# Kernel tuning notes

Hardware: AMD Instinct MI355X
Metric: run time of the kernel (lower is better)

## Reference

```python
import jax, jax.numpy as jnp
import numpy as np

HEADS = 8
EPS = 1e-5


def layernorm(x, g, b):
    mu = jnp.mean(x, axis=-1, keepdims=True)
    var = jnp.mean((x - mu) ** 2, axis=-1, keepdims=True)
    return (x - mu) * jax.lax.rsqrt(var + EPS) * g + b


def setup_inputs() -> dict:
    key = jax.random.key(0)
    ks = jax.random.split(key, 5)
    B, C, H, W = 8, 384, 32, 32
    d = C
    s = 0.02
    return {
        "x": jax.random.normal(ks[0], (B, C, H, W), jnp.float32),
        "ln1_g": jnp.ones((d,), jnp.float32),
        "ln1_b": jnp.zeros((d,), jnp.float32),
        "lna_g": jnp.ones((d,), jnp.float32),
        "lna_b": jnp.zeros((d,), jnp.float32),
        "w_qkv": jax.random.normal(ks[1], (d, 3 * d), jnp.float32) * s,
        "w_out": jax.random.normal(ks[2], (d, d), jnp.float32) * s,
        "ln2_g": jnp.ones((d,), jnp.float32),
        "ln2_b": jnp.zeros((d,), jnp.float32),
        "w1": jax.random.normal(ks[3], (d, 4 * d), jnp.float32) * s,
        "b1": jnp.zeros((4 * d,), jnp.float32),
        "w2": jax.random.normal(ks[4], (4 * d, d), jnp.float32) * s,
        "b2": jnp.zeros((d,), jnp.float32),
    }


def reference(x, ln1_g, ln1_b, lna_g, lna_b, w_qkv, w_out, ln2_g, ln2_b, w1, b1, w2, b2):
    B, C, H, W = x.shape
    d = C
    dh = d // HEADS
    scale = dh ** (-0.5)
    # flatten spatial -> tokens: [B, N, C]
    t = x.reshape(B, C, H * W).transpose(0, 2, 1)

    # --- attention branch (note: double pre-norm, as in original) ---
    a = layernorm(t, ln1_g, ln1_b)
    a = layernorm(a, lna_g, lna_b)
    qkv = a @ w_qkv  # [B, N, 3d]
    q, k, v = jnp.split(qkv, 3, axis=-1)
    q = q.reshape(B, -1, HEADS, dh).transpose(0, 2, 1, 3)  # b h n d
    k = k.reshape(B, -1, HEADS, dh).transpose(0, 2, 1, 3)
    v = v.reshape(B, -1, HEADS, dh).transpose(0, 2, 1, 3)
    dots = jnp.einsum("bhnd,bhmd->bhnm", q, k) * scale
    attn = jax.nn.softmax(dots, axis=-1)
    o = jnp.einsum("bhnm,bhmd->bhnd", attn, v)
    o = o.transpose(0, 2, 1, 3).reshape(B, -1, d)
    t = t + o @ w_out

    # --- MLP branch (exact GELU, as torch nn.GELU default) ---
    m = layernorm(t, ln2_g, ln2_b)
    m = jax.nn.gelu(m @ w1 + b1, approximate=False) @ w2 + b2
    t = t + m

    return t.transpose(0, 2, 1).reshape(B, C, H, W)
```

## Files before the change

kernel.cpp:

```cpp
#include <hip/hip_runtime.h>
#include <math.h>

#define NTOK 1024
#define DM   384
#define NHEAD 8
#define DH   48
#define BATCH 8
#define NROWS (BATCH * NTOK)
#define SC2   (0.14433756729740643f * 1.4426950408889634f)

typedef __attribute__((ext_vector_type(8))) _Float16 f16x8;
typedef __attribute__((ext_vector_type(2))) __fp16 fp16x2_raw;
typedef __attribute__((ext_vector_type(4))) float f32x4;

#define ASYNC16(gp, lp) __builtin_amdgcn_global_load_lds( \
    (const __attribute__((address_space(1))) void*)(gp),  \
    (__attribute__((address_space(3))) void*)(lp), 16, 0, 0)

#define EXP2R(x) __builtin_amdgcn_exp2f(x)
#define RCPR(x)  __builtin_amdgcn_rcpf(x)

__device__ __forceinline__ unsigned int pkh(float a, float b) {
    union { fp16x2_raw h; unsigned int u; } cv;
    cv.h = __builtin_amdgcn_cvt_pkrtz(a, b);
    return cv.u;
}

__device__ __forceinline__ float gelu_fast(float v) {
    const float u = v * (0.7978845608f + 0.0356774081f * v * v);
    const float e = EXP2R(fminf(u * 2.885390082f, 120.0f));
    return v * e * RCPR(e + 1.0f);
}

__global__ __launch_bounds__(256) void prep_kernel(const float* __restrict__ x,
                                                   const float* __restrict__ ln1_g,
                                                   const float* __restrict__ ln1_b,
                                                   const float* __restrict__ lna_g,
                                                   const float* __restrict__ lna_b,
                                                   float* __restrict__ t,
                                                   _Float16* __restrict__ a_h,
                                                   const float* __restrict__ wqkv,
                                                   const float* __restrict__ wout,
                                                   const float* __restrict__ w1,
                                                   const float* __restrict__ w2,
                                                   _Float16* __restrict__ wqkvT,
                                                   _Float16* __restrict__ woutT,
                                                   _Float16* __restrict__ w1T,
                                                   _Float16* __restrict__ w2T) {
    __shared__ float Ts[32][389];
    const int bid = blockIdx.x;
    const int tid = threadIdx.x;

    if (bid >= 256) {
        float (*tile)[33] = (float(*)[33])&Ts[0][0];
        const int wb = bid - 256;
        const float* W; _Float16* Wt; int K, N, nx, tt;
        if (wb < 432)       { W = wqkv; Wt = wqkvT; K = 384;  N = 1152; nx = 36; tt = wb; }
        else if (wb < 576)  { W = wout; Wt = woutT; K = 384;  N = 384;  nx = 12; tt = wb - 432; }
        else if (wb < 1152) { W = w1;   Wt = w1T;   K = 384;  N = 1536; nx = 48; tt = wb - 576; }
        else                { W = w2;   Wt = w2T;   K = 1536; N = 384;  nx = 12; tt = wb - 1152; }
        const int n0 = (tt % nx) * 32, k0 = (tt / nx) * 32;
        const int tx = tid & 31, ty = tid >> 5;
        #pragma unroll
        for (int i = ty; i < 32; i += 8)
            tile[i][tx] = W[(size_t)(k0 + i) * N + n0 + tx];
        __syncthreads();
        #pragma unroll
        for (int i = ty; i < 32; i += 8)
            Wt[(size_t)(n0 + i) * K + k0 + tx] = (_Float16)tile[tx][i];
        return;
    }

    const int b = bid >> 5, n0 = (bid & 31) * 32;
    const int tx = tid & 31, ty8 = tid >> 5;
    const float* xb = x + (size_t)b * (DM * NTOK);
    #pragma unroll
    for (int c0 = 0; c0 < DM; c0 += 32) {
        #pragma unroll
        for (int i = ty8; i < 32; i += 8)
            Ts[tx][c0 + i] = xb[(size_t)(c0 + i) * NTOK + n0 + tx];
    }
    __syncthreads();

    const int g = tid >> 3, sub = tid & 7;
    const int c0 = sub * 48;
    float xv[48];
    #pragma unroll
    for (int k = 0; k < 12; ++k)
        *(float4*)&xv[k * 4] = *(const float4*)&Ts[g][c0 + k * 4];

    const size_t trow = (size_t)((b << 10) + n0 + g) * DM;
    float s = 0.0f, sq = 0.0f;
    #pragma unroll
    for (int k = 0; k < 12; ++k)
        *(float4*)&t[trow + c0 + k * 4] = *(const float4*)&xv[k * 4];
    #pragma unroll
    for (int j = 0; j < 48; ++j) { s += xv[j]; sq += xv[j] * xv[j]; }
    s += __shfl_xor(s, 1, 64); sq += __shfl_xor(sq, 1, 64);
    s += __shfl_xor(s, 2, 64); sq += __shfl_xor(sq, 2, 64);
    s += __shfl_xor(s, 4, 64); sq += __shfl_xor(sq, 4, 64);
    float mu = s * (1.0f / DM);
    float var = fmaxf(sq * (1.0f / DM) - mu * mu, 0.0f);
    float r1 = rsqrtf(var + 1e-5f);

    float s2 = 0.0f, q2 = 0.0f;
    #pragma unroll
    for (int k = 0; k < 12; ++k) {
        const float4 gk = *(const float4*)&ln1_g[c0 + k * 4];
        const float4 bk = *(const float4*)&ln1_b[c0 + k * 4];
        float y0 = (xv[k*4+0] - mu) * r1 * gk.x + bk.x;
        float y1 = (xv[k*4+1] - mu) * r1 * gk.y + bk.y;
        float y2 = (xv[k*4+2] - mu) * r1 * gk.z + bk.z;
        float y3 = (xv[k*4+3] - mu) * r1 * gk.w + bk.w;
        xv[k*4+0] = y0; xv[k*4+1] = y1; xv[k*4+2] = y2; xv[k*4+3] = y3;
        s2 += (y0 + y1) + (y2 + y3);
        q2 += (y0*y0 + y1*y1) + (y2*y2 + y3*y3);
    }
    s2 += __shfl_xor(s2, 1, 64); q2 += __shfl_xor(q2, 1, 64);
    s2 += __shfl_xor(s2, 2, 64); q2 += __shfl_xor(q2, 2, 64);
    s2 += __shfl_xor(s2, 4, 64); q2 += __shfl_xor(q2, 4, 64);
    mu = s2 * (1.0f / DM);
    var = fmaxf(q2 * (1.0f / DM) - mu * mu, 0.0f);
    const float r2 = rsqrtf(var + 1e-5f);

    unsigned int d[12];
    #pragma unroll
    for (int k = 0; k < 12; ++k) {
        const float4 gk = *(const float4*)&lna_g[c0 + k * 4];
        const float4 bk = *(const float4*)&lna_b[c0 + k * 4];
        const float y0 = (xv[k*4+0] - mu) * r2 * gk.x + bk.x;
        const float y1 = (xv[k*4+1] - mu) * r2 * gk.y + bk.y;
        const float y2 = (xv[k*4+2] - mu) * r2 * gk.z + bk.z;
        const float y3 = (xv[k*4+3] - mu) * r2 * gk.w + bk.w;
        d[k*2+0] = pkh(y0, y1); d[k*2+1] = pkh(y2, y3);
    }
    unsigned int* op = (unsigned int*)(a_h + trow + c0);
    #pragma unroll
    for (int k = 0; k < 3; ++k)
        *(uint4*)(op + k * 4) = *(const uint4*)&d[k * 4];
}

template <int EPI, int BN>
__global__ __launch_bounds__(256, 2) void gemm_f16(const _Float16* __restrict__ A,
                                                   const _Float16* __restrict__ Bt,
                                                   const float* __restrict__ bias,
                                                   const float* __restrict__ R,
                                                   _Float16* __restrict__ Ch,
                                                   float* __restrict__ Cf,
                                                   int M, int N, int K) {
    constexpr int NFRAG = BN / 32;
    __shared__ _Float16 As[2][128][64];
    __shared__ _Float16 Bs[2][BN][64];
    const int tid = threadIdx.x;
    const int w = tid >> 6, lane = tid & 63;
    const int l15 = lane & 15, lq = lane >> 4;
    const int bm = blockIdx.y * 128, bn = blockIdx.x * BN;
    const int moff = (w & 1) * 64, noff = (w >> 1) * (BN / 2);

    const int srw = lane >> 3, pp = lane & 7;
    const int c = pp ^ srw;
    const _Float16* Ag[4];
    const _Float16* Bg[NFRAG];
    #pragma unroll
    for (int j = 0; j < 4; ++j)
        Ag[j] = A + (size_t)(bm + w * 32 + j * 8 + srw) * K + c * 8;
    #pragma unroll
    for (int j = 0; j < NFRAG; ++j)
        Bg[j] = Bt + (size_t)(bn + w * (BN / 4) + j * 8 + srw) * K + c * 8;

    const int octA = ((lq ^ (l15 & 7)) << 4);

    f32x4 acc[4][NFRAG];
    #pragma unroll
    for (int mi = 0; mi < 4; ++mi)
        #pragma unroll
        for (int ni = 0; ni < NFRAG; ++ni) acc[mi][ni] = (f32x4){0.f, 0.f, 0.f, 0.f};

    #pragma unroll
    for (int j = 0; j < 4; ++j) { ASYNC16(Ag[j], &As[0][w * 32 + j * 8][0]); Ag[j] += 64; }
    #pragma unroll
    for (int j = 0; j < NFRAG; ++j) { ASYNC16(Bg[j], &Bs[0][w * (BN / 4) + j * 8][0]); Bg[j] += 64; }

    const int nkt = K >> 6;
    for (int kt = 0; kt < nkt; ++kt) {
        const int cur = kt & 1;
        __syncthreads();
        if (kt < nkt - 1) {
            #pragma unroll
            for (int j = 0; j < 4; ++j) { ASYNC16(Ag[j], &As[cur ^ 1][w * 32 + j * 8][0]); Ag[j] += 64; }
            #pragma unroll
            for (int j = 0; j < NFRAG; ++j) { ASYNC16(Bg[j], &Bs[cur ^ 1][w * (BN / 4) + j * 8][0]); Bg[j] += 64; }
        }
        const char* Ab = (const char*)&As[cur][0][0];
        const char* Bb = (const char*)&Bs[cur][0][0];
        #pragma unroll
        for (int ks = 0; ks < 2; ++ks) {
            const int ox = octA ^ (ks << 6);
            f16x8 af[4], bfr[NFRAG];
            #pragma unroll
            for (int mi = 0; mi < 4; ++mi)
                af[mi] = *(const f16x8*)(Ab + ((moff + mi * 16 + l15) << 7) + ox);
            #pragma unroll
            for (int ni = 0; ni < NFRAG; ++ni)
                bfr[ni] = *(const f16x8*)(Bb + ((noff + ni * 16 + l15) << 7) + ox);
            #pragma unroll
            for (int mi = 0; mi < 4; ++mi)
                #pragma unroll
                for (int ni = 0; ni < NFRAG; ++ni)
                    acc[mi][ni] = __builtin_amdgcn_mfma_f32_16x16x32_f16(af[mi], bfr[ni], acc[mi][ni], 0, 0, 0);
        }
    }

    #pragma unroll
    for (int mi = 0; mi < 4; ++mi) {
        #pragma unroll
        for (int ni = 0; ni < NFRAG; ++ni) {
            const int col = bn + noff + ni * 16 + l15;
            float bv = 0.0f;
            if (EPI >= 2) bv = bias[col];
            if (EPI == 4) {
                const int row0 = bm + moff + mi * 16 + lq * 4;
                const int b = row0 >> 10, nn = row0 & 1023;
                float4 vv;
                vv.x = acc[mi][ni][0] + bv + R[(size_t)(row0 + 0) * N + col];
                vv.y = acc[mi][ni][1] + bv + R[(size_t)(row0 + 1) * N + col];
                vv.z = acc[mi][ni][2] + bv + R[(size_t)(row0 + 2) * N + col];
                vv.w = acc[mi][ni][3] + bv + R[(size_t)(row0 + 3) * N + col];
                *(float4*)(Cf + (size_t)b * (DM * NTOK) + (size_t)col * NTOK + nn) = vv;
            } else {
                #pragma unroll
                for (int r = 0; r < 4; ++r) {
                    const int row = bm + moff + mi * 16 + lq * 4 + r;
                    const size_t idx = (size_t)row * N + col;
                    float v = acc[mi][ni][r];
                    if (EPI == 2) v = gelu_fast(v + bv);
                    Ch[idx] = (_Float16)v;
                }
            }
        }
    }
}

__global__ __launch_bounds__(256) void gemm_out_ln(const _Float16* __restrict__ A,
                                                   const _Float16* __restrict__ Bt,
                                                   float* __restrict__ T,
                                                   _Float16* __restrict__ a_out,
                                                   const float* __restrict__ gg,
                                                   const float* __restrict__ bb) {
    __shared__ _Float16 As[2][32][64];
    __shared__ _Float16 Bs[2][384][64];
    __shared__ float red_s[4][16];
    __shared__ float red_q[4][16];
    const int tid = threadIdx.x;
    const int w = tid >> 6, lane = tid & 63;
    const int l15 = lane & 15, lq = lane >> 4;
    const int bm = blockIdx.x * 32;
    const int mr = (w & 1) * 16;
    const int cq = (w >> 1) * 192;

    const int srw = lane >> 3, pp = lane & 7;
    const int c = pp ^ srw;
    const _Float16* Ag = A + (size_t)(bm + w * 8 + srw) * 384 + c * 8;
    const _Float16* Bg[12];
    #pragma unroll
    for (int j = 0; j < 12; ++j)
        Bg[j] = Bt + (size_t)(j * 32 + w * 8 + srw) * 384 + c * 8;

    const int octA = ((lq ^ (l15 & 7)) << 4);

    f32x4 acc[12];
    #pragma unroll
    for (int ni = 0; ni < 12; ++ni) acc[ni] = (f32x4){0.f, 0.f, 0.f, 0.f};

    ASYNC16(Ag, &As[0][w * 8][0]); Ag += 64;
    #pragma unroll
    for (int j = 0; j < 12; ++j) { ASYNC16(Bg[j], &Bs[0][j * 32 + w * 8][0]); Bg[j] += 64; }

    for (int kt = 0; kt < 6; ++kt) {
        const int cur = kt & 1;
        __syncthreads();
        if (kt < 5) {
            ASYNC16(Ag, &As[cur ^ 1][w * 8][0]); Ag += 64;
            #pragma unroll
            for (int j = 0; j < 12; ++j) { ASYNC16(Bg[j], &Bs[cur ^ 1][j * 32 + w * 8][0]); Bg[j] += 64; }
        }
        #pragma unroll
        for (int ks = 0; ks < 2; ++ks) {
            const int ox = octA ^ (ks << 6);
            const f16x8 af = *(const f16x8*)((const char*)&As[cur][0][0] + ((mr + l15) << 7) + ox);
            #pragma unroll
            for (int ni = 0; ni < 12; ++ni) {
                const f16x8 bf = *(const f16x8*)((const char*)&Bs[cur][0][0] + ((cq + ni * 16 + l15) << 7) + ox);
                acc[ni] = __builtin_amdgcn_mfma_f32_16x16x32_f16(af, bf, acc[ni], 0, 0, 0);
            }
        }
    }

    float vv[12][4];
    float s[4] = {0.f, 0.f, 0.f, 0.f}, q[4] = {0.f, 0.f, 0.f, 0.f};
    #pragma unroll
    for (int ni = 0; ni < 12; ++ni) {
        const int col = cq + ni * 16 + l15;
        #pragma unroll
        for (int r = 0; r < 4; ++r) {
            const int row = bm + mr + lq * 4 + r;
            const float v = acc[ni][r] + T[(size_t)row * DM + col];
            vv[ni][r] = v;
            T[(size_t)row * DM + col] = v;
            s[r] += v; q[r] += v * v;
        }
    }
    #pragma unroll
    for (int off = 1; off < 16; off <<= 1) {
        #pragma unroll
        for (int r = 0; r < 4; ++r) {
            s[r] += __shfl_xor(s[r], off, 64);
            q[r] += __shfl_xor(q[r], off, 64);
        }
    }
    if (l15 == 0) {
        #pragma unroll
        for (int r = 0; r < 4; ++r) {
            red_s[w][lq * 4 + r] = s[r];
            red_q[w][lq * 4 + r] = q[r];
        }
    }
    __syncthreads();
    float mu[4], rs[4];
    #pragma unroll
    for (int r = 0; r < 4; ++r) {
        const float ts = s[r] + red_s[w ^ 2][lq * 4 + r];
        const float tq = q[r] + red_q[w ^ 2][lq * 4 + r];
        mu[r] = ts * (1.0f / DM);
        const float var = fmaxf(tq * (1.0f / DM) - mu[r] * mu[r], 0.0f);
        rs[r] = rsqrtf(var + 1e-5f);
    }
    #pragma unroll
    for (int ni = 0; ni < 12; ++ni) {
        const int col = cq + ni * 16 + l15;
        const float gv = gg[col], bv = bb[col];
        #pragma unroll
        for (int r = 0; r < 4; ++r) {
            const int row = bm + mr + lq * 4 + r;
            a_out[(size_t)row * DM + col] = (_Float16)((vv[ni][r] - mu[r]) * rs[r] * gv + bv);
        }
    }
}

__global__ __launch_bounds__(256) void attn_kernel(const _Float16* __restrict__ qkv,
                                                   _Float16* __restrict__ o) {
    __shared__ _Float16 Ks[2][64][64];
    __shared__ _Float16 Vt[2][48][72];
    __shared__ _Float16 Ps[4][16][72];
    const int tid = threadIdx.x;
    const int w = tid >> 6, lane = tid & 63;
    const int l15 = lane & 15, lq = lane >> 4;
    const int bid = blockIdx.x;
    const int bh = ((bid >> 3) & 7) * 8 + (bid & 7);
    const int qt0 = (bid >> 6) * 64;
    const int h = bh & 7, b = bh >> 3;

    const _Float16* qbase = qkv + (size_t)b * NTOK * 1152 + h * 48;
    const _Float16* kbase = qbase + 384;
    const _Float16* vbase = qbase + 768;

    f16x8 qf[2];
    {
        const size_t qrow = (size_t)(qt0 + w * 16 + l15) * 1152;
        qf[0] = *(const f16x8*)(qbase + qrow + lq * 8);
        if (lq < 2) qf[1] = *(const f16x8*)(qbase + qrow + 32 + lq * 8);
        else        qf[1] = (f16x8){(_Float16)0, (_Float16)0, (_Float16)0, (_Float16)0,
                                    (_Float16)0, (_Float16)0, (_Float16)0, (_Float16)0};
    }

    const int srw = lane >> 3, pp = lane & 7;
    const int ck = pp ^ srw;
    const int ckoff = (ck < 6) ? ck * 8 : (ck - 6) * 8;
    const _Float16* Kg = kbase + (size_t)(w * 16 + srw) * 1152 + ckoff;
    const int vtp = tid & 31, vfo = tid >> 5;
    const _Float16* Vg = vbase + (size_t)(vtp * 2) * 1152 + vfo * 8;

    const int octK = ((lq ^ (l15 & 7)) << 4);

    ASYNC16(Kg, &Ks[0][w * 16][0]);
    ASYNC16(Kg + 8 * 1152, &Ks[0][w * 16 + 8][0]);
    Kg += 64 * 1152;
    uint4 va, vb;
    if (vfo < 6) { va = *(const uint4*)Vg; vb = *(const uint4*)(Vg + 1152); }
    Vg += 64 * 1152;

    f32x4 oacc[3];
    float lpart = 0.0f;
    #pragma unroll
    for (int vf = 0; vf < 3; ++vf) oacc[vf] = (f32x4){0.f, 0.f, 0.f, 0.f};

    int cur = 0;
    for (int kt = 0; kt < 16; ++kt) {
        if (vfo < 6) {
            const unsigned short* as = (const unsigned short*)&va;
            const unsigned short* bs = (const unsigned short*)&vb;
            #pragma unroll
            for (int j = 0; j < 8; ++j) {
                const unsigned int dw = (unsigned int)as[j] | ((unsigned int)bs[j] << 16);
                *(unsigned int*)((char*)&Vt[cur][0][0] + (vfo * 8 + j) * 144 + vtp * 4) = dw;
            }
        }
        __syncthreads();
        if (kt < 15) {
            ASYNC16(Kg, &Ks[cur ^ 1][w * 16][0]);
            ASYNC16(Kg + 8 * 1152, &Ks[cur ^ 1][w * 16 + 8][0]);
            Kg += 64 * 1152;
            if (vfo < 6) { va = *(const uint4*)Vg; vb = *(const uint4*)(Vg + 1152); }
            Vg += 64 * 1152;
        }

        f32x4 sacc[4];
        #pragma unroll
        for (int mi = 0; mi < 4; ++mi) sacc[mi] = (f32x4){0.f, 0.f, 0.f, 0.f};
        #pragma unroll
        for (int ks = 0; ks < 2; ++ks) {
            const int ox = octK ^ (ks << 6);
            #pragma unroll
            for (int mi = 0; mi < 4; ++mi) {
                const f16x8 kf = *(const f16x8*)((const char*)&Ks[cur][0][0] + ((mi * 16 + l15) << 7) + ox);
                sacc[mi] = __builtin_amdgcn_mfma_f32_16x16x32_f16(kf, qf[ks], sacc[mi], 0, 0, 0);
            }
        }

        #pragma unroll
        for (int mi = 0; mi < 4; ++mi) {
            const float p0 = EXP2R(sacc[mi][0] * SC2);
            const float p1 = EXP2R(sacc[mi][1] * SC2);
            const float p2 = EXP2R(sacc[mi][2] * SC2);
            const float p3 = EXP2R(sacc[mi][3] * SC2);
            lpart += (p0 + p1) + (p2 + p3);
            uint2 d;
            d.x = pkh(p0, p1); d.y = pkh(p2, p3);
            *(uint2*)((char*)&Ps[w][0][0] + l15 * 144 + (mi * 16 + lq * 4) * 2) = d;
        }
        asm volatile("s_waitcnt lgkmcnt(0)" ::: "memory");

        #pragma unroll
        for (int ks = 0; ks < 2; ++ks) {
            const int kk2 = ks * 64 + lq * 16;
            const f16x8 pf = *(const f16x8*)((const char*)&Ps[w][0][0] + l15 * 144 + kk2);
            #pragma unroll
            for (int vf = 0; vf < 3; ++vf) {
                const f16x8 vv = *(const f16x8*)((const char*)&Vt[cur][0][0] + (vf * 16 + l15) * 144 + kk2);
                oacc[vf] = __builtin_amdgcn_mfma_f32_16x16x32_f16(vv, pf, oacc[vf], 0, 0, 0);
            }
        }
        cur ^= 1;
    }

    lpart += __shfl_xor(lpart, 16, 64);
    lpart += __shfl_xor(lpart, 32, 64);
    const float linv = RCPR(lpart);
    _Float16* ob = o + (size_t)(b * NTOK + qt0 + w * 16 + l15) * DM + h * DH;
    #pragma unroll
    for (int vf = 0; vf < 3; ++vf) {
        uint2 d;
        d.x = pkh(oacc[vf][0] * linv, oacc[vf][1] * linv);
        d.y = pkh(oacc[vf][2] * linv, oacc[vf][3] * linv);
        *(uint2*)(ob + vf * 16 + lq * 4) = d;
    }
}

extern "C" void kernel_launch(void* const* d_in, const int* in_sizes, int n_in,
                              void* d_out, int out_size, void* d_ws, size_t ws_size,
                              hipStream_t stream) {
    const float* x     = (const float*)d_in[0];
    const float* ln1_g = (const float*)d_in[1];
    const float* ln1_b = (const float*)d_in[2];
    const float* lna_g = (const float*)d_in[3];
    const float* lna_b = (const float*)d_in[4];
    const float* w_qkv = (const float*)d_in[5];
    const float* w_out = (const float*)d_in[6];
    const float* ln2_g = (const float*)d_in[7];
    const float* ln2_b = (const float*)d_in[8];
    const float* w1    = (const float*)d_in[9];
    const float* b1    = (const float*)d_in[10];
    const float* w2    = (const float*)d_in[11];
    const float* b2    = (const float*)d_in[12];
    float* out = (float*)d_out;

    char* wsb = (char*)d_ws;
    float* t          = (float*)(wsb);
    _Float16* a_h     = (_Float16*)(wsb + 12582912);
    _Float16* qkv_h   = (_Float16*)(wsb + 18874368);
    _Float16* o_h     = (_Float16*)(wsb + 37748736);
    _Float16* h1_h    = (_Float16*)(wsb + 44040192);
    _Float16* wqkvT   = (_Float16*)(wsb + 69206016);
    _Float16* woutT   = (_Float16*)(wsb + 70090752);
    _Float16* w1T     = (_Float16*)(wsb + 70385664);
    _Float16* w2T     = (_Float16*)(wsb + 71565312);

    prep_kernel<<<256 + 1728, 256, 0, stream>>>(x, ln1_g, ln1_b, lna_g, lna_b, t, a_h,
                                                w_qkv, w_out, w1, w2, wqkvT, woutT, w1T, w2T);
    gemm_f16<0, 192><<<dim3(6, 64), 256, 0, stream>>>(a_h, wqkvT, nullptr, nullptr, qkv_h, nullptr, NROWS, 3 * DM, DM);
    attn_kernel<<<1024, 256, 0, stream>>>(qkv_h, o_h);
    gemm_out_ln<<<256, 256, 0, stream>>>(o_h, woutT, t, a_h, ln2_g, ln2_b);
    gemm_f16<2, 192><<<dim3(8, 64), 256, 0, stream>>>(a_h, w1T, b1, nullptr, h1_h, nullptr, NROWS, 4 * DM, DM);
    gemm_f16<4, 64><<<dim3(6, 64), 256, 0, stream>>>(h1_h, w2T, b2, t, nullptr, out, NROWS, DM, 4 * DM);
}
```

Measured before the change: 219.3 us.

## Fuse out-projection, LayerNorm and full MLP into one tail kernel

Replaces the out-projection+LN kernel and the two MLP GEMM launches with a single kernel. Each 32-row block keeps the normalized activations and a 384-wide GELU hidden chunk in LDS and accumulates the down-projection in registers. This removes the global write and read of the hidden activation and the t residual round trip, plus two launches. In exchange, every block re-streams all of W1 and W2 with a small M tile and uses large LDS, which limits occupancy to one block per CU.

```diff
diff --git a/kernel.cpp b/kernel.cpp
--- a/kernel.cpp
+++ b/kernel.cpp
@@ -140,13 +140,10 @@
         *(uint4*)(op + k * 4) = *(const uint4*)&d[k * 4];
 }
 
-template <int EPI, int BN>
+template <int BN>
 __global__ __launch_bounds__(256, 2) void gemm_f16(const _Float16* __restrict__ A,
                                                    const _Float16* __restrict__ Bt,
-                                                   const float* __restrict__ bias,
-                                                   const float* __restrict__ R,
                                                    _Float16* __restrict__ Ch,
-                                                   float* __restrict__ Cf,
                                                    int M, int N, int K) {
     constexpr int NFRAG = BN / 32;
     __shared__ _Float16 As[2][128][64];
@@ -216,73 +213,65 @@
         #pragma unroll
         for (int ni = 0; ni < NFRAG; ++ni) {
             const int col = bn + noff + ni * 16 + l15;
-            float bv = 0.0f;
-            if (EPI >= 2) bv = bias[col];
-            if (EPI == 4) {
-                const int row0 = bm + moff + mi * 16 + lq * 4;
-                const int b = row0 >> 10, nn = row0 & 1023;
-                float4 vv;
-                vv.x = acc[mi][ni][0] + bv + R[(size_t)(row0 + 0) * N + col];
-                vv.y = acc[mi][ni][1] + bv + R[(size_t)(row0 + 1) * N + col];
-                vv.z = acc[mi][ni][2] + bv + R[(size_t)(row0 + 2) * N + col];
-                vv.w = acc[mi][ni][3] + bv + R[(size_t)(row0 + 3) * N + col];
-                *(float4*)(Cf + (size_t)b * (DM * NTOK) + (size_t)col * NTOK + nn) = vv;
-            } else {
-                #pragma unroll
-                for (int r = 0; r < 4; ++r) {
-                    const int row = bm + moff + mi * 16 + lq * 4 + r;
-                    const size_t idx = (size_t)row * N + col;
-                    float v = acc[mi][ni][r];
-                    if (EPI == 2) v = gelu_fast(v + bv);
-                    Ch[idx] = (_Float16)v;
-                }
-            }
-        }
-    }
-}
-
-__global__ __launch_bounds__(256) void gemm_out_ln(const _Float16* __restrict__ A,
-                                                   const _Float16* __restrict__ Bt,
-                                                   float* __restrict__ T,
-                                                   _Float16* __restrict__ a_out,
+            #pragma unroll
+            for (int r = 0; r < 4; ++r) {
+                const int row = bm + moff + mi * 16 + lq * 4 + r;
+                Ch[(size_t)row * N + col] = (_Float16)acc[mi][ni][r];
+            }
+        }
+    }
+}
+
+__global__ __launch_bounds__(256) void tail_kernel(const _Float16* __restrict__ Oh,
+                                                   const _Float16* __restrict__ WoT,
+                                                   const _Float16* __restrict__ W1T,
+                                                   const _Float16* __restrict__ W2T,
+                                                   const float* __restrict__ T,
+                                                   float* __restrict__ Out,
                                                    const float* __restrict__ gg,
-                                                   const float* __restrict__ bb) {
+                                                   const float* __restrict__ bb,
+                                                   const float* __restrict__ b1v,
+                                                   const float* __restrict__ b2v) {
+    __shared__ _Float16 Bs[2][384][64];
     __shared__ _Float16 As[2][32][64];
-    __shared__ _Float16 Bs[2][384][64];
+    __shared__ _Float16 a_lds[32][392];
+    __shared__ _Float16 hbuf[32][392];
     __shared__ float red_s[4][16];
     __shared__ float red_q[4][16];
+
     const int tid = threadIdx.x;
     const int w = tid >> 6, lane = tid & 63;
     const int l15 = lane & 15, lq = lane >> 4;
     const int bm = blockIdx.x * 32;
     const int mr = (w & 1) * 16;
     const int cq = (w >> 1) * 192;
-
     const int srw = lane >> 3, pp = lane & 7;
-    const int c = pp ^ srw;
-    const _Float16* Ag = A + (size_t)(bm + w * 8 + srw) * 384 + c * 8;
-    const _Float16* Bg[12];
-    #pragma unroll
-    for (int j = 0; j < 12; ++j)
-        Bg[j] = Bt + (size_t)(j * 32 + w * 8 + srw) * 384 + c * 8;
-
+    const int cswz = pp ^ srw;
     const int octA = ((lq ^ (l15 & 7)) << 4);
 
-    f32x4 acc[12];
-    #pragma unroll
-    for (int ni = 0; ni < 12; ++ni) acc[ni] = (f32x4){0.f, 0.f, 0.f, 0.f};
+    auto stageB = [&](int half, const _Float16* base, int rstride, int kofs) {
+        #pragma unroll
+        for (int j = 0; j < 12; ++j)
+            ASYNC16(base + (size_t)(j * 32 + w * 8 + srw) * rstride + kofs + cswz * 8,
+                    &Bs[half][j * 32 + w * 8][0]);
+    };
+
+    const _Float16* Ag = Oh + (size_t)(bm + w * 8 + srw) * 384 + cswz * 8;
+    f32x4 acc1[12];
+    #pragma unroll
+    for (int ni = 0; ni < 12; ++ni) acc1[ni] = (f32x4){0.f, 0.f, 0.f, 0.f};
 
     ASYNC16(Ag, &As[0][w * 8][0]); Ag += 64;
-    #pragma unroll
-    for (int j = 0; j < 12; ++j) { ASYNC16(Bg[j], &Bs[0][j * 32 + w * 8][0]); Bg[j] += 64; }
+    stageB(0, WoT, 384, 0);
 
     for (int kt = 0; kt < 6; ++kt) {
         const int cur = kt & 1;
         __syncthreads();
         if (kt < 5) {
             ASYNC16(Ag, &As[cur ^ 1][w * 8][0]); Ag += 64;
-            #pragma unroll
-            for (int j = 0; j < 12; ++j) { ASYNC16(Bg[j], &Bs[cur ^ 1][j * 32 + w * 8][0]); Bg[j] += 64; }
+            stageB(cur ^ 1, WoT, 384, (kt + 1) * 64);
+        } else {
+            stageB(cur ^ 1, W1T, 384, 0);
         }
         #pragma unroll
         for (int ks = 0; ks < 2; ++ks) {
@@ -291,7 +280,7 @@
             #pragma unroll
             for (int ni = 0; ni < 12; ++ni) {
                 const f16x8 bf = *(const f16x8*)((const char*)&Bs[cur][0][0] + ((cq + ni * 16 + l15) << 7) + ox);
-                acc[ni] = __builtin_amdgcn_mfma_f32_16x16x32_f16(af, bf, acc[ni], 0, 0, 0);
+                acc1[ni] = __builtin_amdgcn_mfma_f32_16x16x32_f16(af, bf, acc1[ni], 0, 0, 0);
             }
         }
     }
@@ -304,9 +293,8 @@
         #pragma unroll
         for (int r = 0; r < 4; ++r) {
             const int row = bm + mr + lq * 4 + r;
-            const float v = acc[ni][r] + T[(size_t)row * DM + col];
+            const float v = acc1[ni][r] + T[(size_t)row * DM + col];
             vv[ni][r] = v;
-            T[(size_t)row * DM + col] = v;
             s[r] += v; q[r] += v * v;
         }
     }
@@ -320,10 +308,7 @@
     }
     if (l15 == 0) {
         #pragma unroll
-        for (int r = 0; r < 4; ++r) {
-            red_s[w][lq * 4 + r] = s[r];
-            red_q[w][lq * 4 + r] = q[r];
-        }
+        for (int r = 0; r < 4; ++r) { red_s[w][lq * 4 + r] = s[r]; red_q[w][lq * 4 + r] = q[r]; }
     }
     __syncthreads();
     float mu[4], rs[4];
@@ -340,10 +325,75 @@
         const int col = cq + ni * 16 + l15;
         const float gv = gg[col], bv = bb[col];
         #pragma unroll
-        for (int r = 0; r < 4; ++r) {
-            const int row = bm + mr + lq * 4 + r;
-            a_out[(size_t)row * DM + col] = (_Float16)((vv[ni][r] - mu[r]) * rs[r] * gv + bv);
-        }
+        for (int r = 0; r < 4; ++r)
+            a_lds[mr + lq * 4 + r][col] = (_Float16)((vv[ni][r] - mu[r]) * rs[r] * gv + bv);
+    }
+
+    f32x4 acc2[12];
+    #pragma unroll
+    for (int ni = 0; ni < 12; ++ni) acc2[ni] = (f32x4){0.f, 0.f, 0.f, 0.f};
+
+    int buf = 0;
+    #pragma unroll 1
+    for (int c = 0; c < 4; ++c) {
+        f32x4 hc[12];
+        #pragma unroll
+        for (int ni = 0; ni < 12; ++ni) hc[ni] = (f32x4){0.f, 0.f, 0.f, 0.f};
+        for (int kt = 0; kt < 6; ++kt) {
+            __syncthreads();
+            if (kt < 5) stageB(buf ^ 1, W1T + (size_t)(c * 384) * 384, 384, (kt + 1) * 64);
+            else        stageB(buf ^ 1, W2T, 1536, c * 384);
+            #pragma unroll
+            for (int ks = 0; ks < 2; ++ks) {
+                const int kk = kt * 64 + ks * 32;
+                const f16x8 af = *(const f16x8*)&a_lds[mr + l15][kk + lq * 8];
+                const int ox = octA ^ (ks << 6);
+                #pragma unroll
+                for (int ni = 0; ni < 12; ++ni) {
+                    const f16x8 bf = *(const f16x8*)((const char*)&Bs[buf][0][0] + ((cq + ni * 16 + l15) << 7) + ox);
+                    hc[ni] = __builtin_amdgcn_mfma_f32_16x16x32_f16(af, bf, hc[ni], 0, 0, 0);
+                }
+            }
+            buf ^= 1;
+        }
+        #pragma unroll
+        for (int ni = 0; ni < 12; ++ni) {
+            const float bv = b1v[c * 384 + cq + ni * 16 + l15];
+            #pragma unroll
+            for (int r = 0; r < 4; ++r)
+                hbuf[mr + lq * 4 + r][cq + ni * 16 + l15] = (_Float16)gelu_fast(hc[ni][r] + bv);
+        }
+        for (int kt = 0; kt < 6; ++kt) {
+            __syncthreads();
+            if (kt < 5)     stageB(buf ^ 1, W2T, 1536, c * 384 + (kt + 1) * 64);
+            else if (c < 3) stageB(buf ^ 1, W1T + (size_t)((c + 1) * 384) * 384, 384, 0);
+            #pragma unroll
+            for (int ks = 0; ks < 2; ++ks) {
+                const int kk = kt * 64 + ks * 32;
+                const f16x8 af = *(const f16x8*)&hbuf[mr + l15][kk + lq * 8];
+                const int ox = octA ^ (ks << 6);
+                #pragma unroll
+                for (int ni = 0; ni < 12; ++ni) {
+                    const f16x8 bf = *(const f16x8*)((const char*)&Bs[buf][0][0] + ((cq + ni * 16 + l15) << 7) + ox);
+                    acc2[ni] = __builtin_amdgcn_mfma_f32_16x16x32_f16(af, bf, acc2[ni], 0, 0, 0);
+                }
+            }
+            buf ^= 1;
+        }
+    }
+
+    #pragma unroll
+    for (int ni = 0; ni < 12; ++ni) {
+        const int col = cq + ni * 16 + l15;
+        const float bv = b2v[col];
+        const int row0 = bm + mr + lq * 4;
+        const int b = row0 >> 10, nn = row0 & 1023;
+        float4 ov;
+        ov.x = acc2[ni][0] + bv + vv[ni][0];
+        ov.y = acc2[ni][1] + bv + vv[ni][1];
+        ov.z = acc2[ni][2] + bv + vv[ni][2];
+        ov.w = acc2[ni][3] + bv + vv[ni][3];
+        *(float4*)(Out + (size_t)b * (DM * NTOK) + (size_t)col * NTOK + nn) = ov;
     }
 }
 
@@ -446,8 +496,8 @@
             const f16x8 pf = *(const f16x8*)((const char*)&Ps[w][0][0] + l15 * 144 + kk2);
             #pragma unroll
             for (int vf = 0; vf < 3; ++vf) {
-                const f16x8 vv = *(const f16x8*)((const char*)&Vt[cur][0][0] + (vf * 16 + l15) * 144 + kk2);
-                oacc[vf] = __builtin_amdgcn_mfma_f32_16x16x32_f16(vv, pf, oacc[vf], 0, 0, 0);
+                const f16x8 vvv = *(const f16x8*)((const char*)&Vt[cur][0][0] + (vf * 16 + l15) * 144 + kk2);
+                oacc[vf] = __builtin_amdgcn_mfma_f32_16x16x32_f16(vvv, pf, oacc[vf], 0, 0, 0);
             }
         }
         cur ^= 1;
@@ -489,7 +539,6 @@
     _Float16* a_h     = (_Float16*)(wsb + 12582912);
     _Float16* qkv_h   = (_Float16*)(wsb + 18874368);
     _Float16* o_h     = (_Float16*)(wsb + 37748736);
-    _Float16* h1_h    = (_Float16*)(wsb + 44040192);
     _Float16* wqkvT   = (_Float16*)(wsb + 69206016);
     _Float16* woutT   = (_Float16*)(wsb + 70090752);
     _Float16* w1T     = (_Float16*)(wsb + 70385664);
@@ -497,9 +546,8 @@
 
     prep_kernel<<<256 + 1728, 256, 0, stream>>>(x, ln1_g, ln1_b, lna_g, lna_b, t, a_h,
                                                 w_qkv, w_out, w1, w2, wqkvT, woutT, w1T, w2T);
-    gemm_f16<0, 192><<<dim3(6, 64), 256, 0, stream>>>(a_h, wqkvT, nullptr, nullptr, qkv_h, nullptr, NROWS, 3 * DM, DM);
+    gemm_f16<192><<<dim3(6, 64), 256, 0, stream>>>(a_h, wqkvT, qkv_h, NROWS, 3 * DM, DM);
     attn_kernel<<<1024, 256, 0, stream>>>(qkv_h, o_h);
-    gemm_out_ln<<<256, 256, 0, stream>>>(o_h, woutT, t, a_h, ln2_g, ln2_b);
-    gemm_f16<2, 192><<<dim3(8, 64), 256, 0, stream>>>(a_h, w1T, b1, nullptr, h1_h, nullptr, NROWS, 4 * DM, DM);
-    gemm_f16<4, 64><<<dim3(6, 64), 256, 0, stream>>>(h1_h, w2T, b2, t, nullptr, out, NROWS, DM, 4 * DM);
-}
+    tail_kernel<<<256, 256, 0, stream>>>(o_h, woutT, w1T, w2T, t, out,
+                                         ln2_g, ln2_b, b1, b2);
+}
```

Measured after the change: 241.5 us. 1.1x slower.

## Replace LDS-tiled GEMM with register-direct MFMA GEMM for QKV and W1 projections

Applied to the files above, without the earlier changes.

Adds a new GEMM kernel that loads A and B fragments straight from global memory into registers, double-buffered across K steps, with no LDS staging or barriers. Each wave computes a 64x96 tile, and the kernel is used for the QKV and first MLP projections (K=384). The goal is to remove LDS traffic and synchronisation overhead. In exchange it gives up cross-wave data sharing, so global loads become uncoalesced strided 16-byte reads that lean on L2/L1, and the epilogue writes are scattered per-element.

```diff
diff --git a/kernel.cpp b/kernel.cpp
--- a/kernel.cpp
+++ b/kernel.cpp
@@ -138,6 +138,84 @@
     #pragma unroll
     for (int k = 0; k < 3; ++k)
         *(uint4*)(op + k * 4) = *(const uint4*)&d[k * 4];
+}
+
+template <int KT, int EPI>
+__global__ __launch_bounds__(256, 2) void rgemm_f16(const _Float16* __restrict__ A,
+                                                    const _Float16* __restrict__ Bt,
+                                                    const float* __restrict__ bias,
+                                                    _Float16* __restrict__ Ch,
+                                                    int N) {
+    const int tid = threadIdx.x;
+    const int w = tid >> 6, lane = tid & 63;
+    const int l15 = lane & 15, lq = lane >> 4;
+    const int bm = blockIdx.x * 256 + w * 64;
+    const int bn = blockIdx.y * 96;
+
+    const _Float16* pA[4];
+    const _Float16* pB[6];
+    #pragma unroll
+    for (int mi = 0; mi < 4; ++mi) pA[mi] = A + (size_t)(bm + mi * 16 + l15) * KT + lq * 8;
+    #pragma unroll
+    for (int ni = 0; ni < 6; ++ni) pB[ni] = Bt + (size_t)(bn + ni * 16 + l15) * KT + lq * 8;
+
+    f32x4 acc[4][6];
+    #pragma unroll
+    for (int mi = 0; mi < 4; ++mi)
+        #pragma unroll
+        for (int ni = 0; ni < 6; ++ni) acc[mi][ni] = (f32x4){0.f, 0.f, 0.f, 0.f};
+
+    constexpr int NS = KT / 32;
+    f16x8 aA[4], bA[6], aB[4], bB[6];
+    #pragma unroll
+    for (int mi = 0; mi < 4; ++mi) aA[mi] = *(const f16x8*)(pA[mi]);
+    #pragma unroll
+    for (int ni = 0; ni < 6; ++ni) bA[ni] = *(const f16x8*)(pB[ni]);
+
+    #pragma unroll
+    for (int s = 0; s < NS; s += 2) {
+        if (s + 1 < NS) {
+            #pragma unroll
+            for (int mi = 0; mi < 4; ++mi) aB[mi] = *(const f16x8*)(pA[mi] + (s + 1) * 32);
+            #pragma unroll
+            for (int ni = 0; ni < 6; ++ni) bB[ni] = *(const f16x8*)(pB[ni] + (s + 1) * 32);
+        }
+        #pragma unroll
+        for (int mi = 0; mi < 4; ++mi)
+            #pragma unroll
+            for (int ni = 0; ni < 6; ++ni)
+                acc[mi][ni] = __builtin_amdgcn_mfma_f32_16x16x32_f16(aA[mi], bA[ni], acc[mi][ni], 0, 0, 0);
+        if (s + 2 < NS) {
+            #pragma unroll
+            for (int mi = 0; mi < 4; ++mi) aA[mi] = *(const f16x8*)(pA[mi] + (s + 2) * 32);
+            #pragma unroll
+            for (int ni = 0; ni < 6; ++ni) bA[ni] = *(const f16x8*)(pB[ni] + (s + 2) * 32);
+        }
+        if (s + 1 < NS) {
+            #pragma unroll
+            for (int mi = 0; mi < 4; ++mi)
+                #pragma unroll
+                for (int ni = 0; ni < 6; ++ni)
+                    acc[mi][ni] = __builtin_amdgcn_mfma_f32_16x16x32_f16(aB[mi], bB[ni], acc[mi][ni], 0, 0, 0);
+        }
+    }
+
+    #pragma unroll
+    for (int mi = 0; mi < 4; ++mi) {
+        #pragma unroll
+        for (int ni = 0; ni < 6; ++ni) {
+            const int col = bn + ni * 16 + l15;
+            float bv = 0.0f;
+            if (EPI == 2) bv = bias[col];
+            #pragma unroll
+            for (int r = 0; r < 4; ++r) {
+                const int row = bm + mi * 16 + lq * 4 + r;
+                float v = acc[mi][ni][r];
+                if (EPI == 2) v = gelu_fast(v + bv);
+                Ch[(size_t)row * N + col] = (_Float16)v;
+            }
+        }
+    }
 }
 
 template <int EPI, int BN>
@@ -446,8 +524,8 @@
             const f16x8 pf = *(const f16x8*)((const char*)&Ps[w][0][0] + l15 * 144 + kk2);
             #pragma unroll
             for (int vf = 0; vf < 3; ++vf) {
-                const f16x8 vv = *(const f16x8*)((const char*)&Vt[cur][0][0] + (vf * 16 + l15) * 144 + kk2);
-                oacc[vf] = __builtin_amdgcn_mfma_f32_16x16x32_f16(vv, pf, oacc[vf], 0, 0, 0);
+                const f16x8 vvv = *(const f16x8*)((const char*)&Vt[cur][0][0] + (vf * 16 + l15) * 144 + kk2);
+                oacc[vf] = __builtin_amdgcn_mfma_f32_16x16x32_f16(vvv, pf, oacc[vf], 0, 0, 0);
             }
         }
         cur ^= 1;
@@ -497,9 +575,9 @@
 
     prep_kernel<<<256 + 1728, 256, 0, stream>>>(x, ln1_g, ln1_b, lna_g, lna_b, t, a_h,
                                                 w_qkv, w_out, w1, w2, wqkvT, woutT, w1T, w2T);
-    gemm_f16<0, 192><<<dim3(6, 64), 256, 0, stream>>>(a_h, wqkvT, nullptr, nullptr, qkv_h, nullptr, NROWS, 3 * DM, DM);
+    rgemm_f16<384, 0><<<dim3(32, 12), 256, 0, stream>>>(a_h, wqkvT, nullptr, qkv_h, 3 * DM);
     attn_kernel<<<1024, 256, 0, stream>>>(qkv_h, o_h);
     gemm_out_ln<<<256, 256, 0, stream>>>(o_h, woutT, t, a_h, ln2_g, ln2_b);
-    gemm_f16<2, 192><<<dim3(8, 64), 256, 0, stream>>>(a_h, w1T, b1, nullptr, h1_h, nullptr, NROWS, 4 * DM, DM);
+    rgemm_f16<384, 2><<<dim3(32, 16), 256, 0, stream>>>(a_h, w1T, b1, h1_h, 4 * DM);
     gemm_f16<4, 64><<<dim3(6, 64), 256, 0, stream>>>(h1_h, w2T, b2, t, nullptr, out, NROWS, DM, 4 * DM);
 }
```

Measured after the change: 256.7 us. 17.0% more time.
